# Kernel optimization log

Measured on AMD Instinct MI355X. Metric: run time of the kernel, lower is better.

## Reference

```python
import jax, jax.numpy as jnp
import numpy as np

N, E, G = 20000, 160000, 32          # nodes, edges, graphs in batch
F_IN, H, P, C = 67, 2048, 1024, 18   # in_feat, hidden_feat, fc2 width, n_classifier
EPS = 1e-5
SLOPE = 0.01  # leaky_relu default negative slope


def setup_inputs() -> dict:
    key = jax.random.key(0)
    ks = jax.random.split(key, 24)
    w = lambda k, shape: (jax.random.normal(k, shape, jnp.float32) * 0.02)
    return {
        "h": jax.random.normal(ks[0], (N, F_IN), jnp.float32),
        "src": jax.random.randint(ks[1], (E,), 0, N),
        "dst": jax.random.randint(ks[2], (E,), 0, N),
        "gids": jnp.sort(jax.random.randint(ks[3], (N,), 0, G)),
        # SAGEConv layers: fc_self, fc_neigh (no per-fc bias), shared bias
        "ws1": w(ks[4], (F_IN, H)), "wn1": w(ks[5], (F_IN, H)), "b1": jnp.zeros((H,), jnp.float32),
        "ws2": w(ks[6], (H, H)),    "wn2": w(ks[7], (H, H)),    "b2": jnp.zeros((H,), jnp.float32),
        "ws3": w(ks[8], (H, H)),    "wn3": w(ks[9], (H, H)),    "b3": jnp.zeros((H,), jnp.float32),
        # batch norms (gamma, beta)
        "g1": jnp.ones((H,), jnp.float32), "be1": jnp.zeros((H,), jnp.float32),
        "g2": jnp.ones((H,), jnp.float32), "be2": jnp.zeros((H,), jnp.float32),
        "g3": jnp.ones((H,), jnp.float32), "be3": jnp.zeros((H,), jnp.float32),
        # MLP head
        "fw1": w(ks[10], (H, H)), "fb1": jnp.zeros((H,), jnp.float32),
        "fw2": w(ks[11], (H, P)), "fb2": jnp.zeros((P,), jnp.float32),
        "fw3": w(ks[12], (P, C)), "fb3": jnp.zeros((C,), jnp.float32),
    }


def _leaky(x):
    return jnp.where(x >= 0, x, SLOPE * x)


def _sage(x, src, dst, w_self, w_neigh, b):
    # DGL SAGEConv 'mean': mean of neighbor (src) features into dst, then linears.
    nsum = jax.ops.segment_sum(x[src], dst, num_segments=N)            # [N, F]
    deg = jax.ops.segment_sum(jnp.ones((E,), x.dtype), dst, num_segments=N)
    neigh = nsum / jnp.maximum(deg, 1.0)[:, None]                      # 0 for isolated
    return x @ w_self + neigh @ w_neigh + b


def _bn(x, gamma, beta):
    m = x.mean(0)
    v = x.var(0)
    return (x - m) * jax.lax.rsqrt(v + EPS) * gamma + beta


def reference(h, src, dst, gids,
              ws1, wn1, b1, g1, be1,
              ws2, wn2, b2, g2, be2,
              ws3, wn3, b3, g3, be3,
              fw1, fb1, fw2, fb2, fw3, fb3):
    x = _leaky(_bn(_sage(h, src, dst, ws1, wn1, b1), g1, be1))
    x = _leaky(_bn(_sage(x, src, dst, ws2, wn2, b2), g2, be2))
    x = _leaky(_bn(_sage(x, src, dst, ws3, wn3, b3), g3, be3))
    # mean pooling per graph
    gsum = jax.ops.segment_sum(x, gids, num_segments=G)                # [G, H]
    cnt = jax.ops.segment_sum(jnp.ones((N,), x.dtype), gids, num_segments=G)
    hg = gsum / jnp.maximum(cnt, 1.0)[:, None]
    # dropouts are identity in eval
    y = _leaky(hg @ fw1 + fb1)
    y = _leaky(y @ fw2 + fb2)
    return y @ fw3 + fb3
```

## Files before the change

kernel.cpp:

```cpp
#include <hip/hip_runtime.h>

typedef unsigned short u16;
typedef __attribute__((ext_vector_type(4))) float f32x4;
typedef __attribute__((ext_vector_type(8))) __bf16 bf16x8;
typedef __attribute__((ext_vector_type(8))) short s16x8;
typedef __attribute__((ext_vector_type(4))) u16 u16x4;

#define N_NODES 20000
#define N_EDGES 160000
#define N_GRAPH 32
#define F_IN 67
#define HID 2048
#define PW 1024
#define NCLS 18
#define MPAD 20096
#define MPAD2 20224
#define K1 192

__device__ __forceinline__ float bf2f(u16 u) {
    unsigned v = ((unsigned)u) << 16;
    float f; __builtin_memcpy(&f, &v, 4); return f;
}
__device__ __forceinline__ u16 f2bf(float f) {
    unsigned u; __builtin_memcpy(&u, &f, 4);
    u = (u + 0x7FFF + ((u >> 16) & 1)) >> 16;
    return (u16)u;
}
__device__ __forceinline__ int imax(int a, int b) { return a > b ? a : b; }

__device__ __forceinline__ void ld16(const u16* gptr, u16* lptr) {
    __builtin_amdgcn_global_load_lds(
        (const __attribute__((address_space(1))) unsigned int*)gptr,
        (__attribute__((address_space(3))) unsigned int*)lptr,
        16, 0, 0);
}

__global__ void k_hist(const int* __restrict__ dst, int* __restrict__ cnt) {
    int e = blockIdx.x * 256 + threadIdx.x;
    if (e < N_EDGES) atomicAdd(&cnt[dst[e]], 1);
}

__global__ void k_scan(const int* __restrict__ cnt, int* __restrict__ rowptr) {
    __shared__ int part[256];
    int t = threadIdx.x;
    const int per = (N_NODES + 255) / 256;
    int base = t * per;
    int s = 0;
    for (int i = 0; i < per; i++) { int idx = base + i; if (idx < N_NODES) s += cnt[idx]; }
    part[t] = s; __syncthreads();
    for (int off = 1; off < 256; off <<= 1) {
        int v = (t >= off) ? part[t - off] : 0;
        __syncthreads();
        part[t] += v;
        __syncthreads();
    }
    int running = (t == 0) ? 0 : part[t - 1];
    for (int i = 0; i < per; i++) {
        int idx = base + i;
        if (idx < N_NODES) { rowptr[idx] = running; running += cnt[idx]; }
    }
    if (t == 255) rowptr[N_NODES] = running;
}

__global__ void k_scatter(const int* __restrict__ src, const int* __restrict__ dst,
                          const int* __restrict__ rowptr, int* __restrict__ cursor,
                          int* __restrict__ csr) {
    int e = blockIdx.x * 256 + threadIdx.x;
    if (e < N_EDGES) {
        int d = dst[e];
        int p = atomicAdd(&cursor[d], 1);
        csr[rowptr[d] + p] = src[e];
    }
}

__global__ void k_w1t(const float* __restrict__ ws1, const float* __restrict__ wn1,
                      u16* __restrict__ w1t) {
    int n = blockIdx.x, t = threadIdx.x;
    float v = 0.f;
    if (t < F_IN) v = ws1[(size_t)t * HID + n];
    else if (t < 2 * F_IN) v = wn1[(size_t)(t - F_IN) * HID + n];
    w1t[(size_t)n * K1 + t] = f2bf(v);
}

__global__ void k_transpose(const float* __restrict__ src, u16* __restrict__ dst, int colofs) {
    __shared__ float tile[32][33];
    int bx = blockIdx.x * 32, by = blockIdx.y * 32;
    int tx = threadIdx.x, ty = threadIdx.y;
#pragma unroll
    for (int i = 0; i < 32; i += 8)
        tile[ty + i][tx] = src[(size_t)(by + ty + i) * HID + bx + tx];
    __syncthreads();
#pragma unroll
    for (int i = 0; i < 32; i += 8)
        dst[(size_t)(bx + ty + i) * (2 * HID) + colofs + by + tx] = f2bf(tile[tx][ty + i]);
}

__global__ void k_agg1(const float* __restrict__ h, const int* __restrict__ rowptr,
                       const int* __restrict__ csr, u16* __restrict__ acat) {
    int n = blockIdx.x, t = threadIdx.x;
    if (t < F_IN) {
        acat[(size_t)n * K1 + t] = f2bf(h[(size_t)n * F_IN + t]);
    } else if (t < 2 * F_IN) {
        int c = t - F_IN;
        int e0 = rowptr[n], e1 = rowptr[n + 1];
        float a = 0.f;
        for (int e = e0; e < e1; e++) a += h[(size_t)csr[e] * F_IN + c];
        acat[(size_t)n * K1 + F_IN + c] = f2bf(a / (float)imax(e1 - e0, 1));
    }
}

__global__ __launch_bounds__(256)
void k_agg(const u16* __restrict__ x, const int* __restrict__ rowptr,
           const int* __restrict__ csr, u16* __restrict__ out) {
    int n = blockIdx.x, t = threadIdx.x;
    int e0 = rowptr[n], e1 = rowptr[n + 1];
    float acc[8] = {0, 0, 0, 0, 0, 0, 0, 0};
    for (int e = e0; e < e1; e++) {
        int s = csr[e];
        s16x8 v = *(const s16x8*)&x[(size_t)s * HID + t * 8];
#pragma unroll
        for (int j = 0; j < 8; j++) acc[j] += bf2f((u16)v[j]);
    }
    float inv = 1.0f / (float)imax(e1 - e0, 1);
    s16x8 o;
#pragma unroll
    for (int j = 0; j < 8; j++) o[j] = (short)f2bf(acc[j] * inv);
    *(s16x8*)&out[(size_t)n * HID + t * 8] = o;
}

__global__ __launch_bounds__(256)
void k_gemm(const u16* __restrict__ A0, const u16* __restrict__ A1, int ksplit,
            const u16* __restrict__ WT, u16* __restrict__ C,
            int ldA, int K, int ldC) {
    __shared__ u16 As[128 * 64];
    __shared__ u16 Bs[128 * 64];
    const int tid = threadIdx.x;
    const int lane = tid & 63;
    const int wave = tid >> 6;
    const int wr = (wave >> 1) * 64;
    const int wc = (wave & 1) * 64;
    const int lr = lane & 15;
    const int lk = (lane >> 4) * 8;
    const size_t row0 = (size_t)blockIdx.x * 128;
    const int col0 = blockIdx.y * 128;

    f32x4 acc[4][4];
#pragma unroll
    for (int i = 0; i < 4; i++)
#pragma unroll
        for (int j = 0; j < 4; j++) acc[i][j] = f32x4{0.f, 0.f, 0.f, 0.f};

    int rr[4], cc[4], lo[4];
#pragma unroll
    for (int i = 0; i < 4; i++) {
        int chunk = i * 256 + tid;
        rr[i] = chunk >> 3;
        cc[i] = (chunk & 7) * 8;
        lo[i] = (i * 256 + (wave << 6)) * 8;
    }
    size_t abase[4], bbase[4];
#pragma unroll
    for (int i = 0; i < 4; i++) {
        abase[i] = (row0 + rr[i]) * (size_t)ldA + cc[i];
        bbase[i] = ((size_t)col0 + rr[i]) * (size_t)K + cc[i];
    }

    for (int kt = 0; kt < K; kt += 64) {
        const u16* Asrc; int kc;
        if (kt < ksplit) { Asrc = A0; kc = kt; } else { Asrc = A1; kc = kt - ksplit; }
#pragma unroll
        for (int i = 0; i < 4; i++) {
            ld16(Asrc + abase[i] + kc, &As[lo[i]]);
            ld16(WT + bbase[i] + kt, &Bs[lo[i]]);
        }
        __syncthreads();
#pragma unroll
        for (int kk = 0; kk < 2; kk++) {
            bf16x8 af[4], bw[4];
#pragma unroll
            for (int i = 0; i < 4; i++)
                af[i] = *(const bf16x8*)&As[(wr + i * 16 + lr) * 64 + kk * 32 + lk];
#pragma unroll
            for (int j = 0; j < 4; j++)
                bw[j] = *(const bf16x8*)&Bs[(wc + j * 16 + lr) * 64 + kk * 32 + lk];
#pragma unroll
            for (int i = 0; i < 4; i++)
#pragma unroll
                for (int j = 0; j < 4; j++)
                    acc[i][j] = __builtin_amdgcn_mfma_f32_16x16x32_bf16(bw[j], af[i], acc[i][j], 0, 0, 0);
        }
        __syncthreads();
    }
#pragma unroll
    for (int i = 0; i < 4; i++) {
        size_t m = row0 + wr + i * 16 + lr;
#pragma unroll
        for (int j = 0; j < 4; j++) {
            int nb = col0 + wc + j * 16 + (lane >> 4) * 4;
            u16x4 o;
#pragma unroll
            for (int rg = 0; rg < 4; rg++) o[rg] = f2bf(acc[i][j][rg]);
            *(u16x4*)&C[m * (size_t)ldC + nb] = o;
        }
    }
}

#define VM4 asm volatile("s_waitcnt vmcnt(4)" ::: "memory")
#define VM2 asm volatile("s_waitcnt vmcnt(2)" ::: "memory")
#define VM0 asm volatile("s_waitcnt vmcnt(0)" ::: "memory")
#define VMNONE asm volatile("" ::: "memory")

#define STAGE_A(H) { const u16* as_ = (kt1 < 32 ? A0 : A1);                        \
    size_t ko_ = (size_t)(kt1 & 31) * 64 + swe;                                     \
    ld16(as_ + (row0 + 0 * 128 + (H) * 64 + r8) * 2048 + ko_,                       \
         LA + dbo + ((H) * 128 + 0 * 64 + r8) * 64 + ld8);                          \
    ld16(as_ + (row0 + 1 * 128 + (H) * 64 + r8) * 2048 + ko_,                       \
         LA + dbo + ((H) * 128 + 1 * 64 + r8) * 64 + ld8); }

#define STAGE_B(H) { size_t ko_ = (size_t)kt1 * 64 + swe;                           \
    ld16(WT + ((size_t)col0 + ((r8 >> 5)) * 64 + (H) * 32 + (r8 & 31)) * 4096 + ko_,\
         LB + dbo + ((H) * 128 + 0 * 64 + r8) * 64 + ld8);                          \
    ld16(WT + ((size_t)col0 + (2 + (r8 >> 5)) * 64 + (H) * 32 + (r8 & 31)) * 4096 + ko_,\
         LB + dbo + ((H) * 128 + 1 * 64 + r8) * 64 + ld8); }

#define RD_A(QM) {                                                                  \
    _Pragma("unroll") for (int f = 0; f < 4; ++f)                                   \
      _Pragma("unroll") for (int kk = 0; kk < 2; ++kk)                              \
        af[f][kk] = *(const bf16x8*)(bA + (QM) * 16384 + (wm * 64 + f * 16 + lr) * 128 \
                                     + ((kk * 64 + lg * 16) ^ rxor)); }

#define RD_B(DST, QN) {                                                             \
    _Pragma("unroll") for (int n = 0; n < 2; ++n)                                   \
      _Pragma("unroll") for (int kk = 0; kk < 2; ++kk)                              \
        DST[n][kk] = *(const bf16x8*)(bB + (QN) * 16384 + (wn * 32 + n * 16 + lr) * 128 \
                                     + ((kk * 64 + lg * 16) ^ rxor)); }

#define SYNC_MM(QM, QN, BW) {                                                       \
    __builtin_amdgcn_s_barrier();                                                   \
    asm volatile("s_waitcnt lgkmcnt(0)" ::: "memory");                              \
    __builtin_amdgcn_sched_barrier(0);                                              \
    __builtin_amdgcn_s_setprio(1);                                                  \
    _Pragma("unroll") for (int kk = 0; kk < 2; ++kk)                                \
      _Pragma("unroll") for (int f = 0; f < 4; ++f)                                 \
        _Pragma("unroll") for (int n = 0; n < 2; ++n)                               \
          acc[(QM) * 4 + f][(QN) * 2 + n] = __builtin_amdgcn_mfma_f32_16x16x32_bf16(\
              BW[n][kk], af[f][kk], acc[(QM) * 4 + f][(QN) * 2 + n], 0, 0, 0);      \
    __builtin_amdgcn_s_setprio(0); }

__global__ __launch_bounds__(512, 2)
void k_gemm256(const u16* __restrict__ A0, const u16* __restrict__ A1,
               const u16* __restrict__ WT, u16* __restrict__ C) {
    __shared__ u16 LA[2 * 256 * 64];
    __shared__ u16 LB[2 * 256 * 64];
    const int tid = threadIdx.x;
    const int lane = tid & 63;
    const int wave = tid >> 6;
    const int wm = wave >> 2, wn = wave & 3;
    const int lr = lane & 15, lg = lane >> 4;
    const int rxor = (lr & 7) << 4;

    const int f2 = (blockIdx.x & 7) * 79 + (blockIdx.x >> 3);
    const size_t row0 = (size_t)(f2 % 79) * 256;
    const int col0 = (f2 / 79) * 256;

    const int r8 = tid >> 3;
    const int ld8 = (tid & 7) * 8;
    const int swe = ((ld8 * 2) ^ ((r8 & 7) << 4)) >> 1;

    f32x4 acc[8][4];
#pragma unroll
    for (int i = 0; i < 8; i++)
#pragma unroll
        for (int j = 0; j < 4; j++) acc[i][j] = f32x4{0.f, 0.f, 0.f, 0.f};

    {
        const int kt1 = 0; const int dbo = 0;
        STAGE_A(0) STAGE_B(0) STAGE_B(1) STAGE_A(1)
    }
    VM0;
    __builtin_amdgcn_s_barrier();

    bf16x8 af[4][2], bw[2][2], bw2[2][2];

    for (int t = 0; t < 63; ++t) {
        const char* bA = (const char*)LA + (t & 1) * 32768;
        const char* bB = (const char*)LB + (t & 1) * 32768;
        const int kt1 = t + 1;
        const int dbo = ((t + 1) & 1) * 16384;
        RD_A(0) RD_B(bw, 0) STAGE_A(0) VM4; SYNC_MM(0, 0, bw)
        RD_B(bw2, 1) STAGE_B(0) VM4; SYNC_MM(0, 1, bw2)
        RD_A(1) STAGE_B(1) SYNC_MM(1, 1, bw2)
        RD_B(bw, 0) STAGE_A(1) VM4; SYNC_MM(1, 0, bw)
    }
    {
        const char* bA = (const char*)LA + 32768;
        const char* bB = (const char*)LB + 32768;
        RD_A(0) RD_B(bw, 0) VM2; SYNC_MM(0, 0, bw)
        RD_B(bw2, 1) VM0; SYNC_MM(0, 1, bw2)
        RD_A(1) SYNC_MM(1, 1, bw2)
        RD_B(bw, 0) SYNC_MM(1, 0, bw)
    }

#pragma unroll
    for (int f = 0; f < 8; ++f) {
        size_t m = row0 + wm * 128 + f * 16 + lr;
#pragma unroll
        for (int n = 0; n < 4; ++n) {
            int cb = col0 + wn * 64 + n * 16 + lg * 4;
            u16x4 o;
#pragma unroll
            for (int rg = 0; rg < 4; ++rg) o[rg] = f2bf(acc[f][n][rg]);
            *(u16x4*)&C[m * HID + cb] = o;
        }
    }
}

__global__ __launch_bounds__(256)
void k_stats(const u16* __restrict__ x, float* __restrict__ ssum, float* __restrict__ ssq) {
    int t = threadIdx.x;
    int r0 = blockIdx.x * 100;
    float s[8] = {}, s2[8] = {};
    for (int i = 0; i < 100; ++i) {
        s16x8 v = *(const s16x8*)&x[(size_t)(r0 + i) * HID + t * 8];
#pragma unroll
        for (int j = 0; j < 8; ++j) { float f = bf2f((u16)v[j]); s[j] += f; s2[j] += f * f; }
    }
#pragma unroll
    for (int j = 0; j < 8; ++j) {
        atomicAdd(&ssum[t * 8 + j], s[j]);
        atomicAdd(&ssq[t * 8 + j], s2[j]);
    }
}

__global__ void k_bnfin(const float* __restrict__ ssum, const float* __restrict__ ssq,
                        const float* __restrict__ gma, const float* __restrict__ bta,
                        float* __restrict__ aco, float* __restrict__ dco) {
    int c = blockIdx.x * 256 + threadIdx.x;
    float m = ssum[c] * (1.0f / N_NODES);
    float v = ssq[c] * (1.0f / N_NODES) - m * m;
    float a = gma[c] * rsqrtf(v + 1e-5f);
    aco[c] = a;
    dco[c] = bta[c] - m * a;
}

__global__ void k_bnleaky(const u16* __restrict__ xin, const float* __restrict__ aco,
                          const float* __restrict__ dco, u16* __restrict__ xout) {
    size_t eb = ((size_t)blockIdx.x * 256 + threadIdx.x) * 8;
    int col = (int)(eb & (HID - 1));
    s16x8 v = *(const s16x8*)&xin[eb];
    s16x8 o;
#pragma unroll
    for (int j = 0; j < 8; j++) {
        float f = bf2f((u16)v[j]) * aco[col + j] + dco[col + j];
        f = f > 0.f ? f : 0.01f * f;
        o[j] = (short)f2bf(f);
    }
    *(s16x8*)&xout[eb] = o;
}

__global__ void k_bounds(const int* __restrict__ gids, int* __restrict__ gstart) {
    int t = threadIdx.x;
    if (t > N_GRAPH) return;
    int lo = 0, hi = N_NODES;
    while (lo < hi) { int mid = (lo + hi) >> 1; if (gids[mid] < t) lo = mid + 1; else hi = mid; }
    gstart[t] = lo;
}

__global__ void k_pool(const u16* __restrict__ x, const int* __restrict__ gstart,
                       float* __restrict__ hg) {
    int g = blockIdx.x;
    int col = blockIdx.y * 256 + threadIdx.x;
    int r0 = gstart[g], r1 = gstart[g + 1];
    float s = 0.f;
    for (int r = r0; r < r1; r++) s += bf2f(x[(size_t)r * HID + col]);
    hg[(size_t)g * HID + col] = s / (float)imax(r1 - r0, 1);
}

__global__ __launch_bounds__(256)
void k_mlp_part(const float* __restrict__ X, const float* __restrict__ W,
                float* __restrict__ Yp, int K, int Nc) {
    __shared__ float xs[32 * 256];
    int t = threadIdx.x;
    int kc = blockIdx.y;
    int n = blockIdx.x * 64 + (t & 63);
    int mg = t >> 6;
#pragma unroll
    for (int l = 0; l < 32; ++l) {
        int e = l * 256 + t;
        xs[e] = X[(size_t)(e >> 8) * K + kc * 256 + (e & 255)];
    }
    __syncthreads();
    float acc[8] = {};
    for (int k = 0; k < 256; ++k) {
        float wv = W[(size_t)(kc * 256 + k) * Nc + n];
#pragma unroll
        for (int i = 0; i < 8; ++i) acc[i] += xs[(mg * 8 + i) * 256 + k] * wv;
    }
#pragma unroll
    for (int i = 0; i < 8; ++i)
        Yp[(size_t)(kc * 32 + mg * 8 + i) * Nc + n] = acc[i];
}

__global__ void k_mlp_red(const float* __restrict__ Yp, const float* __restrict__ bias,
                          float* __restrict__ Y, int Nc, int leaky) {
    int idx = blockIdx.x * 256 + threadIdx.x;
    int n = idx % Nc;
    float s = 0.f;
#pragma unroll
    for (int kc = 0; kc < 8; ++kc) s += Yp[(size_t)kc * 32 * Nc + idx];
    float v = s + bias[n];
    if (leaky) v = v > 0.f ? v : 0.01f * v;
    Y[idx] = v;
}

__global__ void k_fc3(const float* __restrict__ y2, const float* __restrict__ fw3,
                      const float* __restrict__ fb3, float* __restrict__ out) {
    __shared__ float red[8][32];
    int m = blockIdx.x, t = threadIdx.x;
    int ch = t >> 5, c = t & 31;
    float s = 0.f;
    if (c < NCLS) {
        for (int j = 0; j < 128; ++j) {
            int k = ch * 128 + j;
            s += y2[(size_t)m * PW + k] * fw3[(size_t)k * NCLS + c];
        }
    }
    red[ch][c] = s;
    __syncthreads();
    if (t < NCLS) {
        float a = 0.f;
#pragma unroll
        for (int c2 = 0; c2 < 8; ++c2) a += red[c2][t];
        out[m * NCLS + t] = a + fb3[t];
    }
}

extern "C" void kernel_launch(void* const* d_in, const int* in_sizes, int n_in,
                              void* d_out, int out_size, void* d_ws, size_t ws_size,
                              hipStream_t stream) {
    const float* h   = (const float*)d_in[0];
    const int* src   = (const int*)d_in[1];
    const int* dst   = (const int*)d_in[2];
    const int* gids  = (const int*)d_in[3];
    const float* ws1 = (const float*)d_in[4];
    const float* wn1 = (const float*)d_in[5];
    const float* ws2 = (const float*)d_in[7];
    const float* wn2 = (const float*)d_in[8];
    const float* ws3 = (const float*)d_in[10];
    const float* wn3 = (const float*)d_in[11];
    const float* g1  = (const float*)d_in[13];
    const float* be1 = (const float*)d_in[14];
    const float* g2  = (const float*)d_in[15];
    const float* be2 = (const float*)d_in[16];
    const float* g3  = (const float*)d_in[17];
    const float* be3 = (const float*)d_in[18];
    const float* fw1 = (const float*)d_in[19];
    const float* fb1 = (const float*)d_in[20];
    const float* fw2 = (const float*)d_in[21];
    const float* fb2 = (const float*)d_in[22];
    const float* fw3 = (const float*)d_in[23];
    const float* fb3 = (const float*)d_in[24];
    float* out = (float*)d_out;
    (void)in_sizes; (void)n_in; (void)out_size;

    char* base = (char*)d_ws;
    size_t off = 0;
    auto alloc = [&](size_t b) -> char* {
        char* p = base + off;
        off += (b + 255) & ~(size_t)255;
        return p;
    };
    u16* BUF0 = (u16*)alloc((size_t)MPAD2 * HID * 2);
    u16* BUF1 = (u16*)alloc((size_t)MPAD2 * HID * 2);
    u16* BUF2 = (u16*)alloc((size_t)MPAD2 * HID * 2);
    u16* WT   = (u16*)alloc((size_t)HID * 2 * HID * 2);
    int* cnt    = (int*)alloc(N_NODES * 4);
    int* rowptr = (int*)alloc((N_NODES + 1) * 4);
    int* cursor = (int*)alloc(N_NODES * 4);
    int* csr    = (int*)alloc(N_EDGES * 4);
    float* ssum = (float*)alloc(HID * 4);
    float* ssq  = (float*)alloc(HID * 4);
    float* aco  = (float*)alloc(HID * 4);
    float* dco  = (float*)alloc(HID * 4);
    int* gstart = (int*)alloc(64 * 4);
    float* hg = (float*)alloc((size_t)N_GRAPH * HID * 4);
    float* y1 = (float*)alloc((size_t)N_GRAPH * HID * 4);
    float* y2 = (float*)alloc((size_t)N_GRAPH * PW * 4);
    u16* ACAT = (u16*)((char*)BUF2);
    u16* W1T  = (u16*)((char*)BUF2 + (size_t)MPAD * K1 * 2);
    float* Yp = (float*)((char*)BUF2);

    if (off > ws_size) return;

    hipMemsetAsync(cnt, 0, N_NODES * 4, stream);
    hipMemsetAsync(cursor, 0, N_NODES * 4, stream);
    hipMemsetAsync(ACAT, 0, (size_t)MPAD * K1 * 2, stream);

    k_hist<<<(N_EDGES + 255) / 256, 256, 0, stream>>>(dst, cnt);
    k_scan<<<1, 256, 0, stream>>>(cnt, rowptr);
    k_scatter<<<(N_EDGES + 255) / 256, 256, 0, stream>>>(src, dst, rowptr, cursor, csr);

    k_w1t<<<HID, K1, 0, stream>>>(ws1, wn1, W1T);
    k_agg1<<<N_NODES, 192, 0, stream>>>(h, rowptr, csr, ACAT);

    dim3 gg(MPAD / 128, HID / 128);
    dim3 tb(32, 8);
    k_gemm<<<gg, 256, 0, stream>>>(ACAT, ACAT, K1, W1T, BUF0, K1, K1, HID);
    hipMemsetAsync(ssum, 0, 2 * HID * 4, stream);
    k_stats<<<200, 256, 0, stream>>>(BUF0, ssum, ssq);
    k_bnfin<<<HID / 256, 256, 0, stream>>>(ssum, ssq, g1, be1, aco, dco);
    k_bnleaky<<<20000, 256, 0, stream>>>(BUF0, aco, dco, BUF1);
    k_transpose<<<dim3(64, 64), tb, 0, stream>>>(ws2, WT, 0);
    k_transpose<<<dim3(64, 64), tb, 0, stream>>>(wn2, WT, HID);
    k_agg<<<N_NODES, 256, 0, stream>>>(BUF1, rowptr, csr, BUF2);
    k_gemm256<<<632, 512, 0, stream>>>(BUF1, BUF2, WT, BUF0);
    hipMemsetAsync(ssum, 0, 2 * HID * 4, stream);
    k_stats<<<200, 256, 0, stream>>>(BUF0, ssum, ssq);
    k_bnfin<<<HID / 256, 256, 0, stream>>>(ssum, ssq, g2, be2, aco, dco);
    k_bnleaky<<<20000, 256, 0, stream>>>(BUF0, aco, dco, BUF1);
    k_transpose<<<dim3(64, 64), tb, 0, stream>>>(ws3, WT, 0);
    k_transpose<<<dim3(64, 64), tb, 0, stream>>>(wn3, WT, HID);
    k_agg<<<N_NODES, 256, 0, stream>>>(BUF1, rowptr, csr, BUF2);
    k_gemm256<<<632, 512, 0, stream>>>(BUF1, BUF2, WT, BUF0);
    hipMemsetAsync(ssum, 0, 2 * HID * 4, stream);
    k_stats<<<200, 256, 0, stream>>>(BUF0, ssum, ssq);
    k_bnfin<<<HID / 256, 256, 0, stream>>>(ssum, ssq, g3, be3, aco, dco);
    k_bnleaky<<<20000, 256, 0, stream>>>(BUF0, aco, dco, BUF1);
    k_bounds<<<1, 64, 0, stream>>>(gids, gstart);
    k_pool<<<dim3(N_GRAPH, HID / 256), 256, 0, stream>>>(BUF1, gstart, hg);
    k_mlp_part<<<dim3(HID / 64, 8), 256, 0, stream>>>(hg, fw1, Yp, HID, HID);
    k_mlp_red<<<(N_GRAPH * HID) / 256, 256, 0, stream>>>(Yp, fb1, y1, HID, 1);
    k_mlp_part<<<dim3(PW / 64, 8), 256, 0, stream>>>(y1, fw2, Yp, HID, PW);
    k_mlp_red<<<(N_GRAPH * PW) / 256, 256, 0, stream>>>(Yp, fb2, y2, PW, 1);
    k_fc3<<<N_GRAPH, 256, 0, stream>>>(y2, fw3, fb3, out);
}
```

Before: 1.530 ms.

## Shrink big GEMM tile to 128x256 and restructure the LDS pipeline

```diff
diff --git a/kernel.cpp b/kernel.cpp
--- a/kernel.cpp
+++ b/kernel.cpp
@@ -206,51 +206,45 @@
 }
 
 #define VM4 asm volatile("s_waitcnt vmcnt(4)" ::: "memory")
-#define VM2 asm volatile("s_waitcnt vmcnt(2)" ::: "memory")
 #define VM0 asm volatile("s_waitcnt vmcnt(0)" ::: "memory")
-#define VMNONE asm volatile("" ::: "memory")
-
-#define STAGE_A(H) { const u16* as_ = (kt1 < 32 ? A0 : A1);                        \
-    size_t ko_ = (size_t)(kt1 & 31) * 64 + swe;                                     \
-    ld16(as_ + (row0 + 0 * 128 + (H) * 64 + r8) * 2048 + ko_,                       \
-         LA + dbo + ((H) * 128 + 0 * 64 + r8) * 64 + ld8);                          \
-    ld16(as_ + (row0 + 1 * 128 + (H) * 64 + r8) * 2048 + ko_,                       \
-         LA + dbo + ((H) * 128 + 1 * 64 + r8) * 64 + ld8); }
-
-#define STAGE_B(H) { size_t ko_ = (size_t)kt1 * 64 + swe;                           \
-    ld16(WT + ((size_t)col0 + ((r8 >> 5)) * 64 + (H) * 32 + (r8 & 31)) * 4096 + ko_,\
-         LB + dbo + ((H) * 128 + 0 * 64 + r8) * 64 + ld8);                          \
-    ld16(WT + ((size_t)col0 + (2 + (r8 >> 5)) * 64 + (H) * 32 + (r8 & 31)) * 4096 + ko_,\
-         LB + dbo + ((H) * 128 + 1 * 64 + r8) * 64 + ld8); }
-
-#define RD_A(QM) {                                                                  \
-    _Pragma("unroll") for (int f = 0; f < 4; ++f)                                   \
-      _Pragma("unroll") for (int kk = 0; kk < 2; ++kk)                              \
-        af[f][kk] = *(const bf16x8*)(bA + (QM) * 16384 + (wm * 64 + f * 16 + lr) * 128 \
-                                     + ((kk * 64 + lg * 16) ^ rxor)); }
-
-#define RD_B(DST, QN) {                                                             \
-    _Pragma("unroll") for (int n = 0; n < 2; ++n)                                   \
-      _Pragma("unroll") for (int kk = 0; kk < 2; ++kk)                              \
-        DST[n][kk] = *(const bf16x8*)(bB + (QN) * 16384 + (wn * 32 + n * 16 + lr) * 128 \
-                                     + ((kk * 64 + lg * 16) ^ rxor)); }
-
-#define SYNC_MM(QM, QN, BW) {                                                       \
-    __builtin_amdgcn_s_barrier();                                                   \
-    asm volatile("s_waitcnt lgkmcnt(0)" ::: "memory");                              \
-    __builtin_amdgcn_sched_barrier(0);                                              \
-    __builtin_amdgcn_s_setprio(1);                                                  \
-    _Pragma("unroll") for (int kk = 0; kk < 2; ++kk)                                \
-      _Pragma("unroll") for (int f = 0; f < 4; ++f)                                 \
-        _Pragma("unroll") for (int n = 0; n < 2; ++n)                               \
-          acc[(QM) * 4 + f][(QN) * 2 + n] = __builtin_amdgcn_mfma_f32_16x16x32_bf16(\
-              BW[n][kk], af[f][kk], acc[(QM) * 4 + f][(QN) * 2 + n], 0, 0, 0);      \
-    __builtin_amdgcn_s_setprio(0); }
+
+#define STAGE_A() { const u16* as_ = (kt1 < 32 ? A0 : A1);                          \
+    size_t ko_ = (size_t)(kt1 & 31) * 64 + swe;                                      \
+    int g0_ = ((r8 & 32) << 1) | (r8 & 31);                                          \
+    ld16(as_ + (row0 + g0_) * 2048 + ko_, LA + dboA + r8 * 64 + ld8);                \
+    ld16(as_ + (row0 + g0_ + 32) * 2048 + ko_, LA + dboA + (64 + r8) * 64 + ld8); }
+
+#define STAGE_B(H) { size_t ko_ = (size_t)kt1 * 64 + swe;                            \
+    int c0_ = ((r8 >> 5) << 6) + ((H) << 5) + (r8 & 31);                             \
+    ld16(WT + ((size_t)col0 + c0_) * 4096 + ko_,                                     \
+         LB + dboB + ((H) * 128 + r8) * 64 + ld8);                                   \
+    ld16(WT + ((size_t)col0 + c0_ + 128) * 4096 + ko_,                               \
+         LB + dboB + ((H) * 128 + 64 + r8) * 64 + ld8); }
+
+#define RD_A(QM) { _Pragma("unroll") for (int fh = 0; fh < 2; ++fh)                  \
+    _Pragma("unroll") for (int kk = 0; kk < 2; ++kk)                                 \
+      af[fh][kk] = *(const bf16x8*)(bA + ((QM) * 64 + wm * 32 + fh * 16 + lr) * 128  \
+                                    + ((kk * 64 + lg * 16) ^ rxor)); }
+
+#define RD_B(DST, QN) { _Pragma("unroll") for (int n = 0; n < 2; ++n)                \
+    _Pragma("unroll") for (int kk = 0; kk < 2; ++kk)                                 \
+      DST[n][kk] = *(const bf16x8*)(bB + ((QN) * 128 + wn * 32 + n * 16 + lr) * 128  \
+                                    + ((kk * 64 + lg * 16) ^ rxor)); }
+
+#define SYNCIN { __builtin_amdgcn_s_barrier();                                       \
+    asm volatile("s_waitcnt lgkmcnt(0)" ::: "memory");                               \
+    __builtin_amdgcn_sched_barrier(0); }
+
+#define MM8(QM, QN, BW) { _Pragma("unroll") for (int kk = 0; kk < 2; ++kk)           \
+    _Pragma("unroll") for (int fh = 0; fh < 2; ++fh)                                 \
+      _Pragma("unroll") for (int n = 0; n < 2; ++n)                                  \
+        acc[(QM) * 2 + fh][(QN) * 2 + n] = __builtin_amdgcn_mfma_f32_16x16x32_bf16(  \
+            BW[n][kk], af[fh][kk], acc[(QM) * 2 + fh][(QN) * 2 + n], 0, 0, 0); }
 
 __global__ __launch_bounds__(512, 2)
 void k_gemm256(const u16* __restrict__ A0, const u16* __restrict__ A1,
                const u16* __restrict__ WT, u16* __restrict__ C) {
-    __shared__ u16 LA[2 * 256 * 64];
+    __shared__ u16 LA[2 * 128 * 64];
     __shared__ u16 LB[2 * 256 * 64];
     const int tid = threadIdx.x;
     const int lane = tid & 63;
@@ -259,57 +253,76 @@
     const int lr = lane & 15, lg = lane >> 4;
     const int rxor = (lr & 7) << 4;
 
-    const int f2 = (blockIdx.x & 7) * 79 + (blockIdx.x >> 3);
-    const size_t row0 = (size_t)(f2 % 79) * 256;
-    const int col0 = (f2 / 79) * 256;
+    const int f2 = (blockIdx.x & 7) * 158 + (blockIdx.x >> 3);
+    const size_t row0 = (size_t)(f2 % 158) * 128;
+    const int col0 = (f2 / 158) * 256;
 
     const int r8 = tid >> 3;
     const int ld8 = (tid & 7) * 8;
     const int swe = ((ld8 * 2) ^ ((r8 & 7) << 4)) >> 1;
 
-    f32x4 acc[8][4];
-#pragma unroll
-    for (int i = 0; i < 8; i++)
+    f32x4 acc[4][4];
+#pragma unroll
+    for (int i = 0; i < 4; i++)
 #pragma unroll
         for (int j = 0; j < 4; j++) acc[i][j] = f32x4{0.f, 0.f, 0.f, 0.f};
 
     {
-        const int kt1 = 0; const int dbo = 0;
-        STAGE_A(0) STAGE_B(0) STAGE_B(1) STAGE_A(1)
+        const int kt1 = 0; const int dboA = 0; const int dboB = 0;
+        STAGE_B(0) STAGE_B(1) STAGE_A()
     }
     VM0;
     __builtin_amdgcn_s_barrier();
 
-    bf16x8 af[4][2], bw[2][2], bw2[2][2];
+    bf16x8 af[2][2], bw[2][2], bw2[2][2];
 
     for (int t = 0; t < 63; ++t) {
-        const char* bA = (const char*)LA + (t & 1) * 32768;
+        const char* bA = (const char*)LA + (t & 1) * 16384;
         const char* bB = (const char*)LB + (t & 1) * 32768;
         const int kt1 = t + 1;
-        const int dbo = ((t + 1) & 1) * 16384;
-        RD_A(0) RD_B(bw, 0) STAGE_A(0) VM4; SYNC_MM(0, 0, bw)
-        RD_B(bw2, 1) STAGE_B(0) VM4; SYNC_MM(0, 1, bw2)
-        RD_A(1) STAGE_B(1) SYNC_MM(1, 1, bw2)
-        RD_B(bw, 0) STAGE_A(1) VM4; SYNC_MM(1, 0, bw)
+        const int dboA = ((t + 1) & 1) * 8192;
+        const int dboB = ((t + 1) & 1) * 16384;
+        RD_A(0) RD_B(bw, 0) STAGE_B(0) STAGE_B(1) VM4;
+        SYNCIN
+        __builtin_amdgcn_s_setprio(1);
+        MM8(0, 0, bw)
+        __builtin_amdgcn_s_setprio(0);
+        RD_B(bw2, 1) STAGE_A()
+        SYNCIN
+        __builtin_amdgcn_s_setprio(1);
+        MM8(0, 1, bw2)
+        __builtin_amdgcn_s_setprio(0);
+        RD_A(1)
+        SYNCIN
+        __builtin_amdgcn_s_setprio(1);
+        MM8(1, 1, bw2)
+        MM8(1, 0, bw)
+        __builtin_amdgcn_s_setprio(0);
     }
     {
-        const char* bA = (const char*)LA + 32768;
+        const char* bA = (const char*)LA + 16384;
         const char* bB = (const char*)LB + 32768;
-        RD_A(0) RD_B(bw, 0) VM2; SYNC_MM(0, 0, bw)
-        RD_B(bw2, 1) VM0; SYNC_MM(0, 1, bw2)
-        RD_A(1) SYNC_MM(1, 1, bw2)
-        RD_B(bw, 0) SYNC_MM(1, 0, bw)
-    }
-
-#pragma unroll
-    for (int f = 0; f < 8; ++f) {
-        size_t m = row0 + wm * 128 + f * 16 + lr;
-#pragma unroll
-        for (int n = 0; n < 4; ++n) {
-            int cb = col0 + wn * 64 + n * 16 + lg * 4;
+        RD_A(0) RD_B(bw, 0) VM0;
+        SYNCIN
+        MM8(0, 0, bw)
+        RD_B(bw2, 1)
+        SYNCIN
+        MM8(0, 1, bw2)
+        RD_A(1)
+        SYNCIN
+        MM8(1, 1, bw2)
+        MM8(1, 0, bw)
+    }
+
+#pragma unroll
+    for (int i = 0; i < 4; ++i) {
+        size_t m = row0 + wm * 64 + i * 16 + lr;
+#pragma unroll
+        for (int j = 0; j < 4; ++j) {
+            int cb = col0 + wn * 64 + j * 16 + lg * 4;
             u16x4 o;
 #pragma unroll
-            for (int rg = 0; rg < 4; ++rg) o[rg] = f2bf(acc[f][n][rg]);
+            for (int rg = 0; rg < 4; ++rg) o[rg] = f2bf(acc[i][j][rg]);
             *(u16x4*)&C[m * HID + cb] = o;
         }
     }
@@ -513,7 +526,7 @@
     k_transpose<<<dim3(64, 64), tb, 0, stream>>>(ws2, WT, 0);
     k_transpose<<<dim3(64, 64), tb, 0, stream>>>(wn2, WT, HID);
     k_agg<<<N_NODES, 256, 0, stream>>>(BUF1, rowptr, csr, BUF2);
-    k_gemm256<<<632, 512, 0, stream>>>(BUF1, BUF2, WT, BUF0);
+    k_gemm256<<<1264, 512, 0, stream>>>(BUF1, BUF2, WT, BUF0);
     hipMemsetAsync(ssum, 0, 2 * HID * 4, stream);
     k_stats<<<200, 256, 0, stream>>>(BUF0, ssum, ssq);
     k_bnfin<<<HID / 256, 256, 0, stream>>>(ssum, ssq, g2, be2, aco, dco);
@@ -521,7 +534,7 @@
     k_transpose<<<dim3(64, 64), tb, 0, stream>>>(ws3, WT, 0);
     k_transpose<<<dim3(64, 64), tb, 0, stream>>>(wn3, WT, HID);
     k_agg<<<N_NODES, 256, 0, stream>>>(BUF1, rowptr, csr, BUF2);
-    k_gemm256<<<632, 512, 0, stream>>>(BUF1, BUF2, WT, BUF0);
+    k_gemm256<<<1264, 512, 0, stream>>>(BUF1, BUF2, WT, BUF0);
     hipMemsetAsync(ssum, 0, 2 * HID * 4, stream);
     k_stats<<<200, 256, 0, stream>>>(BUF0, ssum, ssq);
     k_bnfin<<<HID / 256, 256, 0, stream>>>(ssum, ssq, g3, be3, aco, dco);
```

Measured after the change: 1.641 ms. 1.07x slower.

## Load GEMM B operand directly from global into registers, drop B LDS staging

Applied to the files above, without the earlier changes.

```diff
diff --git a/kernel.cpp b/kernel.cpp
--- a/kernel.cpp
+++ b/kernel.cpp
@@ -205,10 +205,10 @@
     }
 }
 
-#define VM4 asm volatile("s_waitcnt vmcnt(4)" ::: "memory")
-#define VM2 asm volatile("s_waitcnt vmcnt(2)" ::: "memory")
-#define VM0 asm volatile("s_waitcnt vmcnt(0)" ::: "memory")
-#define VMNONE asm volatile("" ::: "memory")
+#define VMC10 asm volatile("s_waitcnt vmcnt(10)" ::: "memory")
+#define VMC2  asm volatile("s_waitcnt vmcnt(2)" ::: "memory")
+#define VMC0  asm volatile("s_waitcnt vmcnt(0)" ::: "memory")
+#define WNONE asm volatile("" ::: "memory")
 
 #define STAGE_A(H) { const u16* as_ = (kt1 < 32 ? A0 : A1);                        \
     size_t ko_ = (size_t)(kt1 & 31) * 64 + swe;                                     \
@@ -217,11 +217,12 @@
     ld16(as_ + (row0 + 1 * 128 + (H) * 64 + r8) * 2048 + ko_,                       \
          LA + dbo + ((H) * 128 + 1 * 64 + r8) * 64 + ld8); }
 
-#define STAGE_B(H) { size_t ko_ = (size_t)kt1 * 64 + swe;                           \
-    ld16(WT + ((size_t)col0 + ((r8 >> 5)) * 64 + (H) * 32 + (r8 & 31)) * 4096 + ko_,\
-         LB + dbo + ((H) * 128 + 0 * 64 + r8) * 64 + ld8);                          \
-    ld16(WT + ((size_t)col0 + (2 + (r8 >> 5)) * 64 + (H) * 32 + (r8 & 31)) * 4096 + ko_,\
-         LB + dbo + ((H) * 128 + 1 * 64 + r8) * 64 + ld8); }
+#define LOAD_B(DST, KT) {                                                           \
+    _Pragma("unroll") for (int qn = 0; qn < 2; ++qn)                                \
+      _Pragma("unroll") for (int n = 0; n < 2; ++n)                                 \
+        _Pragma("unroll") for (int kk = 0; kk < 2; ++kk)                            \
+          DST[qn][n][kk] = *(const bf16x8*)&WT[bwrow + (size_t)(qn * 32 + n * 16) * 4096 \
+                                               + (size_t)(KT) * 64 + kk * 32 + lg * 8]; }
 
 #define RD_A(QM) {                                                                  \
     _Pragma("unroll") for (int f = 0; f < 4; ++f)                                   \
@@ -229,29 +230,42 @@
         af[f][kk] = *(const bf16x8*)(bA + (QM) * 16384 + (wm * 64 + f * 16 + lr) * 128 \
                                      + ((kk * 64 + lg * 16) ^ rxor)); }
 
-#define RD_B(DST, QN) {                                                             \
-    _Pragma("unroll") for (int n = 0; n < 2; ++n)                                   \
-      _Pragma("unroll") for (int kk = 0; kk < 2; ++kk)                              \
-        DST[n][kk] = *(const bf16x8*)(bB + (QN) * 16384 + (wn * 32 + n * 16 + lr) * 128 \
-                                     + ((kk * 64 + lg * 16) ^ rxor)); }
-
-#define SYNC_MM(QM, QN, BW) {                                                       \
-    __builtin_amdgcn_s_barrier();                                                   \
-    asm volatile("s_waitcnt lgkmcnt(0)" ::: "memory");                              \
-    __builtin_amdgcn_sched_barrier(0);                                              \
-    __builtin_amdgcn_s_setprio(1);                                                  \
+#define MM32(QM, BW) {                                                              \
     _Pragma("unroll") for (int kk = 0; kk < 2; ++kk)                                \
       _Pragma("unroll") for (int f = 0; f < 4; ++f)                                 \
-        _Pragma("unroll") for (int n = 0; n < 2; ++n)                               \
-          acc[(QM) * 4 + f][(QN) * 2 + n] = __builtin_amdgcn_mfma_f32_16x16x32_bf16(\
-              BW[n][kk], af[f][kk], acc[(QM) * 4 + f][(QN) * 2 + n], 0, 0, 0);      \
-    __builtin_amdgcn_s_setprio(0); }
+        _Pragma("unroll") for (int qn = 0; qn < 2; ++qn)                            \
+          _Pragma("unroll") for (int n = 0; n < 2; ++n)                             \
+            acc[(QM) * 4 + f][qn * 2 + n] = __builtin_amdgcn_mfma_f32_16x16x32_bf16(\
+                BW[qn][n][kk], af[f][kk], acc[(QM) * 4 + f][qn * 2 + n], 0, 0, 0); }
+
+#define SYNCIN { __builtin_amdgcn_s_barrier();                                      \
+    asm volatile("s_waitcnt lgkmcnt(0)" ::: "memory");                              \
+    __builtin_amdgcn_sched_barrier(0); }
+
+#define TILE_BODY(T, CUR, NXT, DO_STAGE, WA, WB) {                                  \
+    const char* bA = (const char*)LA + ((T) & 1) * 32768;                           \
+    const int kt1 = (T) + 1;                                                        \
+    const int dbo = (((T) + 1) & 1) * 16384;                                        \
+    RD_A(0)                                                                         \
+    if (DO_STAGE) { STAGE_A(0) LOAD_B(NXT, kt1) }                                   \
+    WA;                                                                             \
+    SYNCIN                                                                          \
+    __builtin_amdgcn_s_setprio(1);                                                  \
+    MM32(0, CUR)                                                                    \
+    __builtin_amdgcn_s_setprio(0);                                                  \
+    RD_A(1)                                                                         \
+    if (DO_STAGE) { STAGE_A(1) }                                                    \
+    WB;                                                                             \
+    SYNCIN                                                                          \
+    __builtin_amdgcn_s_setprio(1);                                                  \
+    MM32(1, CUR)                                                                    \
+    __builtin_amdgcn_s_setprio(0);                                                  \
+}
 
 __global__ __launch_bounds__(512, 2)
 void k_gemm256(const u16* __restrict__ A0, const u16* __restrict__ A1,
                const u16* __restrict__ WT, u16* __restrict__ C) {
     __shared__ u16 LA[2 * 256 * 64];
-    __shared__ u16 LB[2 * 256 * 64];
     const int tid = threadIdx.x;
     const int lane = tid & 63;
     const int wave = tid >> 6;
@@ -266,40 +280,29 @@
     const int r8 = tid >> 3;
     const int ld8 = (tid & 7) * 8;
     const int swe = ((ld8 * 2) ^ ((r8 & 7) << 4)) >> 1;
+    const size_t bwrow = ((size_t)col0 + wn * 64 + lr) * 4096;
 
     f32x4 acc[8][4];
 #pragma unroll
     for (int i = 0; i < 8; i++)
 #pragma unroll
         for (int j = 0; j < 4; j++) acc[i][j] = f32x4{0.f, 0.f, 0.f, 0.f};
+
+    bf16x8 af[4][2], bwE[2][2][2], bwO[2][2][2];
 
     {
         const int kt1 = 0; const int dbo = 0;
-        STAGE_A(0) STAGE_B(0) STAGE_B(1) STAGE_A(1)
-    }
-    VM0;
+        STAGE_A(0) LOAD_B(bwE, 0) STAGE_A(1)
+    }
+    VMC0;
     __builtin_amdgcn_s_barrier();
 
-    bf16x8 af[4][2], bw[2][2], bw2[2][2];
-
-    for (int t = 0; t < 63; ++t) {
-        const char* bA = (const char*)LA + (t & 1) * 32768;
-        const char* bB = (const char*)LB + (t & 1) * 32768;
-        const int kt1 = t + 1;
-        const int dbo = ((t + 1) & 1) * 16384;
-        RD_A(0) RD_B(bw, 0) STAGE_A(0) VM4; SYNC_MM(0, 0, bw)
-        RD_B(bw2, 1) STAGE_B(0) VM4; SYNC_MM(0, 1, bw2)
-        RD_A(1) STAGE_B(1) SYNC_MM(1, 1, bw2)
-        RD_B(bw, 0) STAGE_A(1) VM4; SYNC_MM(1, 0, bw)
-    }
-    {
-        const char* bA = (const char*)LA + 32768;
-        const char* bB = (const char*)LB + 32768;
-        RD_A(0) RD_B(bw, 0) VM2; SYNC_MM(0, 0, bw)
-        RD_B(bw2, 1) VM0; SYNC_MM(0, 1, bw2)
-        RD_A(1) SYNC_MM(1, 1, bw2)
-        RD_B(bw, 0) SYNC_MM(1, 0, bw)
-    }
+    for (int t = 0; t < 62; t += 2) {
+        TILE_BODY(t, bwE, bwO, 1, VMC10, VMC2)
+        TILE_BODY(t + 1, bwO, bwE, 1, VMC10, VMC2)
+    }
+    TILE_BODY(62, bwE, bwO, 1, VMC10, VMC2)
+    TILE_BODY(63, bwO, bwE, 0, VMC0, WNONE)
 
 #pragma unroll
     for (int f = 0; f < 8; ++f) {
@@ -348,12 +351,20 @@
     size_t eb = ((size_t)blockIdx.x * 256 + threadIdx.x) * 8;
     int col = (int)(eb & (HID - 1));
     s16x8 v = *(const s16x8*)&xin[eb];
+    f32x4 a0 = *(const f32x4*)&aco[col], a1 = *(const f32x4*)&aco[col + 4];
+    f32x4 d0 = *(const f32x4*)&dco[col], d1 = *(const f32x4*)&dco[col + 4];
     s16x8 o;
 #pragma unroll
-    for (int j = 0; j < 8; j++) {
-        float f = bf2f((u16)v[j]) * aco[col + j] + dco[col + j];
+    for (int j = 0; j < 4; j++) {
+        float f = bf2f((u16)v[j]) * a0[j] + d0[j];
         f = f > 0.f ? f : 0.01f * f;
         o[j] = (short)f2bf(f);
+    }
+#pragma unroll
+    for (int j = 0; j < 4; j++) {
+        float f = bf2f((u16)v[4 + j]) * a1[j] + d1[j];
+        f = f > 0.f ? f : 0.01f * f;
+        o[4 + j] = (short)f2bf(f);
     }
     *(s16x8*)&xout[eb] = o;
 }
```

Result: slower. 1.972 ms (+28.8%).
